# Optimization experiments

Measured on AMD Instinct MI355X. Metric: run time of the kernel, lower is better.

The kernel has to match this reference:

```python
import jax, jax.numpy as jnp
import numpy as np


def setup_inputs() -> dict:
    key = jax.random.key(0)
    k1, k2 = jax.random.split(key)
    x = jax.random.normal(k1, (16384, 4096), dtype=jnp.float32)
    # parameter initialized uniform(-0.01, 0.01) in the original
    v = jax.random.uniform(k2, (4096, 256), dtype=jnp.float32, minval=-0.01, maxval=0.01)
    return {"x": x, "v": v}


def reference(x, v):
    # FM second-order term: sum_{i<j} (v_i . v_j) x_i x_j
    # = 0.5 * (||x @ v||^2 - sum_f (x^2 @ v^2)_f), per batch row.
    xv = jnp.einsum('bn,nf->bf', x, v)            # [B, F]
    x2v2 = jnp.einsum('bn,nf->bf', x * x, v * v)  # [B, F]
    res = 0.5 * jnp.sum(xv * xv - x2v2, axis=-1, keepdims=True)  # [B, 1]
    return res
```

## Files before the change

kernel.cpp:

```cpp
#include <hip/hip_runtime.h>
#include <hip/hip_bf16.h>

#define B_DIM 16384
#define K_DIM 4096
#define F_DIM 256
#define BM 32
#define BK 64
#define NSTEP (K_DIM / BK)

typedef short bf16x8 __attribute__((ext_vector_type(8)));
typedef float f32x4 __attribute__((ext_vector_type(4)));

static __device__ __forceinline__ ushort f2bf(float f) {
    union { __hip_bfloat16 h; ushort s; } u;
    u.h = __float2bfloat16(f);
    return u.s;
}

static __device__ __forceinline__ void gload_lds16(const void* g, void* l) {
    __builtin_amdgcn_global_load_lds(
        (const __attribute__((address_space(1))) unsigned int*)g,
        (__attribute__((address_space(3))) unsigned int*)l, 16, 0, 0);
}

__global__ __launch_bounds__(512) void prep_w(const float* __restrict__ v,
                                              float* __restrict__ w) {
    const int lane = threadIdx.x & 63;
    const int n = blockIdx.x * 8 + (threadIdx.x >> 6);
    const float4 vv = *reinterpret_cast<const float4*>(v + (size_t)n * F_DIM + lane * 4);
    float s = vv.x * vv.x + vv.y * vv.y + vv.z * vv.z + vv.w * vv.w;
#pragma unroll
    for (int m = 1; m < 64; m <<= 1) s += __shfl_xor(s, m);
    if (lane == 0) w[n] = s;
}

__global__ __launch_bounds__(512) void prep_t(const float* __restrict__ v,
                                              ushort* __restrict__ vT) {
    __shared__ ushort T[256][72];
    const int tid = threadIdx.x;
    const int n0 = blockIdx.x * 64;
    const int wid = tid >> 6;
    const int f0 = (tid & 63) * 4;
#pragma unroll
    for (int j = 0; j < 8; ++j) {
        const int r = j * 8 + wid;
        const float4 vv = *reinterpret_cast<const float4*>(v + (size_t)(n0 + r) * F_DIM + f0);
        T[f0 + 0][r] = f2bf(vv.x);
        T[f0 + 1][r] = f2bf(vv.y);
        T[f0 + 2][r] = f2bf(vv.z);
        T[f0 + 3][r] = f2bf(vv.w);
    }
    __syncthreads();
    const int nb = (tid & 7) * 8;
#pragma unroll
    for (int s = 0; s < 4; ++s) {
        const int f = s * 64 + (tid >> 3);
        const uint4 val = *reinterpret_cast<const uint4*>(&T[f][nb]);
        *reinterpret_cast<uint4*>(vT + (size_t)f * K_DIM + n0 + nb) = val;
    }
}

__global__ __launch_bounds__(256, 3) void fm_kernel(const float* __restrict__ x,
                                                    const ushort* __restrict__ vT,
                                                    const float* __restrict__ w,
                                                    float* __restrict__ out) {
    __shared__ float Ab[2][BM * BK];
    __shared__ float red[BM][4];
    __shared__ float s2red[BM];

    const int tid = threadIdx.x;
    const int lane = tid & 63;
    const int wc = tid >> 6;
    const int l15 = lane & 15;
    const int koff = lane >> 4;

    const int mbase = blockIdx.x * BM;

    const int srow = tid >> 4;
    const int sj = (tid & 15) * 16;
    const int sjj = sj ^ ((srow & 7) << 4);
    const float* gx1 = x + (size_t)(mbase + srow) * K_DIM + (sjj >> 2);
    const float* gx2 = x + (size_t)(mbase + 16 + srow) * K_DIM + (sjj >> 2);

    auto stageA = [&](int k0, int buf) {
        char* base = reinterpret_cast<char*>(&Ab[buf][0]) + wc * 1024;
        gload_lds16(gx1 + k0, base);
        gload_lds16(gx2 + k0, base + 4096);
    };

    int aRo[2], aXm[2];
#pragma unroll
    for (int m = 0; m < 2; ++m) {
        const int r = m * 16 + l15;
        aRo[m] = r * 256;
        aXm[m] = (r & 7) << 4;
    }
    const int cbase = koff * 32;

    const ushort* vb = vT + (size_t)(wc * 64 + l15) * K_DIM + koff * 8;
    const float* wb = w + koff * 8;

    f32x4 acc[2][4] = {};
    float s2m0 = 0.f, s2m1 = 0.f;
    bf16x8 bA[4][2], bB[4][2];

    auto loadB = [&](int k0, bf16x8 (&bn)[4][2]) {
#pragma unroll
        for (int n = 0; n < 4; ++n)
#pragma unroll
            for (int ks = 0; ks < 2; ++ks)
                bn[n][ks] = *reinterpret_cast<const bf16x8*>(
                    vb + (size_t)n * 16 * K_DIM + k0 + ks * 32);
    };

    auto compute = [&](int k0, int buf, bf16x8 (&bc)[4][2]) {
        const char* Ac = reinterpret_cast<const char*>(&Ab[buf][0]);
        bf16x8 af[2][2];
#pragma unroll
        for (int ks = 0; ks < 2; ++ks) {
            float4 wlo = {0, 0, 0, 0}, whi = {0, 0, 0, 0};
            if (wc == 0) {
                wlo = *reinterpret_cast<const float4*>(wb + k0 + ks * 32);
                whi = *reinterpret_cast<const float4*>(wb + k0 + ks * 32 + 4);
            }
#pragma unroll
            for (int m = 0; m < 2; ++m) {
                const int c0 = (ks * 128 + cbase) ^ aXm[m];
                const int c1 = (ks * 128 + cbase + 16) ^ aXm[m];
                const f32x4 lo = *reinterpret_cast<const f32x4*>(Ac + aRo[m] + c0);
                const f32x4 hi = *reinterpret_cast<const f32x4*>(Ac + aRo[m] + c1);
                bf16x8 a;
                a[0] = (short)f2bf(lo[0]); a[1] = (short)f2bf(lo[1]);
                a[2] = (short)f2bf(lo[2]); a[3] = (short)f2bf(lo[3]);
                a[4] = (short)f2bf(hi[0]); a[5] = (short)f2bf(hi[1]);
                a[6] = (short)f2bf(hi[2]); a[7] = (short)f2bf(hi[3]);
                af[m][ks] = a;
                if (wc == 0) {
                    const float t = lo[0] * lo[0] * wlo.x + lo[1] * lo[1] * wlo.y
                                  + lo[2] * lo[2] * wlo.z + lo[3] * lo[3] * wlo.w
                                  + hi[0] * hi[0] * whi.x + hi[1] * hi[1] * whi.y
                                  + hi[2] * hi[2] * whi.z + hi[3] * hi[3] * whi.w;
                    if (m == 0) s2m0 += t; else s2m1 += t;
                }
            }
        }
#pragma unroll
        for (int ks = 0; ks < 2; ++ks)
#pragma unroll
            for (int m = 0; m < 2; ++m)
#pragma unroll
                for (int n = 0; n < 4; ++n)
                    acc[m][n] = __builtin_amdgcn_mfma_f32_16x16x32_bf16(
                        af[m][ks], bc[n][ks], acc[m][n], 0, 0, 0);
    };

    stageA(0, 0);
    loadB(0, bA);
    __syncthreads();

    for (int t = 0; t < NSTEP; t += 2) {
        stageA((t + 1) * BK, 1);
        loadB((t + 1) * BK, bB);
        compute(t * BK, 0, bA);
        __syncthreads();
        if (t + 2 < NSTEP) {
            stageA((t + 2) * BK, 0);
            loadB((t + 2) * BK, bA);
        }
        compute((t + 1) * BK, 1, bB);
        __syncthreads();
    }

#pragma unroll
    for (int m = 0; m < 2; ++m) {
#pragma unroll
        for (int j = 0; j < 4; ++j) {
            float s = 0.f;
#pragma unroll
            for (int n = 0; n < 4; ++n) { const float y = acc[m][n][j]; s += y * y; }
            s += __shfl_xor(s, 1);
            s += __shfl_xor(s, 2);
            s += __shfl_xor(s, 4);
            s += __shfl_xor(s, 8);
            if (l15 == 0) red[m * 16 + koff * 4 + j][wc] = s;
        }
    }
    if (wc == 0) {
        s2m0 += __shfl_xor(s2m0, 16); s2m0 += __shfl_xor(s2m0, 32);
        s2m1 += __shfl_xor(s2m1, 16); s2m1 += __shfl_xor(s2m1, 32);
        if (lane < 16) { s2red[lane] = s2m0; s2red[16 + lane] = s2m1; }
    }
    __syncthreads();
    if (tid < BM) {
        out[mbase + tid] = 0.5f * (red[tid][0] + red[tid][1] + red[tid][2]
                                   + red[tid][3] - s2red[tid]);
    }
}

extern "C" void kernel_launch(void* const* d_in, const int* in_sizes, int n_in,
                              void* d_out, int out_size, void* d_ws, size_t ws_size,
                              hipStream_t stream) {
    const float* x = (const float*)d_in[0];
    const float* v = (const float*)d_in[1];
    float* out = (float*)d_out;

    ushort* vT = (ushort*)d_ws;
    float* w = (float*)((char*)d_ws + (size_t)F_DIM * K_DIM * sizeof(ushort));

    prep_w<<<K_DIM / 8, 512, 0, stream>>>(v, w);
    prep_t<<<K_DIM / 64, 512, 0, stream>>>(v, vT);
    fm_kernel<<<B_DIM / BM, 256, 0, stream>>>(x, vT, w, out);
}
```

Measured before the change: 472.4 us.

## Stage A tile through registers as bf16 and spread x²·w work across all waves

Drops the direct global-to-LDS fp32 loads. Each thread now loads its x slice and w into registers two steps ahead, computes the x²·w partial sum, converts x to bf16 and writes packed, swizzled bf16 into LDS. The MFMA loop then reads bf16 fragments straight from LDS with no conversion, and the diagonal-term work is split over all four waves instead of only wave 0. In exchange it uses more registers for the prefetch buffers, and launch bounds drop occupancy from 3 to 2 blocks per SM; it also replaces __syncthreads with a manual waitcnt plus barrier.

```diff
diff --git a/kernel.cpp b/kernel.cpp
--- a/kernel.cpp
+++ b/kernel.cpp
@@ -15,12 +15,6 @@
     union { __hip_bfloat16 h; ushort s; } u;
     u.h = __float2bfloat16(f);
     return u.s;
-}
-
-static __device__ __forceinline__ void gload_lds16(const void* g, void* l) {
-    __builtin_amdgcn_global_load_lds(
-        (const __attribute__((address_space(1))) unsigned int*)g,
-        (__attribute__((address_space(3))) unsigned int*)l, 16, 0, 0);
 }
 
 __global__ __launch_bounds__(512) void prep_w(const float* __restrict__ v,
@@ -60,11 +54,14 @@
     }
 }
 
-__global__ __launch_bounds__(256, 3) void fm_kernel(const float* __restrict__ x,
+struct APend { float4 xa, xb, wa, wb; };
+struct BReg { bf16x8 v[4][2]; };
+
+__global__ __launch_bounds__(256, 2) void fm_kernel(const float* __restrict__ x,
                                                     const ushort* __restrict__ vT,
                                                     const float* __restrict__ w,
                                                     float* __restrict__ out) {
-    __shared__ float Ab[2][BM * BK];
+    __shared__ ushort As[2][BM * BK];
     __shared__ float red[BM][4];
     __shared__ float s2red[BM];
 
@@ -73,77 +70,64 @@
     const int wc = tid >> 6;
     const int l15 = lane & 15;
     const int koff = lane >> 4;
-
     const int mbase = blockIdx.x * BM;
 
-    const int srow = tid >> 4;
-    const int sj = (tid & 15) * 16;
-    const int sjj = sj ^ ((srow & 7) << 4);
-    const float* gx1 = x + (size_t)(mbase + srow) * K_DIM + (sjj >> 2);
-    const float* gx2 = x + (size_t)(mbase + 16 + srow) * K_DIM + (sjj >> 2);
-
-    auto stageA = [&](int k0, int buf) {
-        char* base = reinterpret_cast<char*>(&Ab[buf][0]) + wc * 1024;
-        gload_lds16(gx1 + k0, base);
-        gload_lds16(gx2 + k0, base + 4096);
-    };
-
-    int aRo[2], aXm[2];
-#pragma unroll
-    for (int m = 0; m < 2; ++m) {
-        const int r = m * 16 + l15;
-        aRo[m] = r * 256;
-        aXm[m] = (r & 7) << 4;
-    }
-    const int cbase = koff * 32;
-
+    const int srow = tid >> 3;
+    const int kb = (tid & 7) * 8;
+    const float* px = x + (size_t)(mbase + srow) * K_DIM + kb;
+    const float* pw = w + kb;
+    const int wbyte = srow * 128 + (((tid & 7) * 16) ^ ((srow & 7) << 4));
+
+    int aoff[2][2];
+#pragma unroll
+    for (int m = 0; m < 2; ++m)
+#pragma unroll
+        for (int ks = 0; ks < 2; ++ks)
+            aoff[m][ks] = (m * 16 + l15) * 128
+                        + ((koff * 16 + ks * 64) ^ ((l15 & 7) << 4));
     const ushort* vb = vT + (size_t)(wc * 64 + l15) * K_DIM + koff * 8;
-    const float* wb = w + koff * 8;
-
+
+    float s2 = 0.f;
     f32x4 acc[2][4] = {};
-    float s2m0 = 0.f, s2m1 = 0.f;
-    bf16x8 bA[4][2], bB[4][2];
-
-    auto loadB = [&](int k0, bf16x8 (&bn)[4][2]) {
+    APend p0, p1;
+    BReg b0, b1;
+
+    auto loadA = [&](int t, APend& p) {
+        const int k0 = (t < NSTEP ? t : NSTEP - 1) * BK;
+        p.xa = *reinterpret_cast<const float4*>(px + k0);
+        p.xb = *reinterpret_cast<const float4*>(px + k0 + 4);
+        p.wa = *reinterpret_cast<const float4*>(pw + k0);
+        p.wb = *reinterpret_cast<const float4*>(pw + k0 + 4);
+    };
+    auto loadB = [&](int t, BReg& b) {
+        const int k0 = (t < NSTEP ? t : NSTEP - 1) * BK;
 #pragma unroll
         for (int n = 0; n < 4; ++n)
 #pragma unroll
             for (int ks = 0; ks < 2; ++ks)
-                bn[n][ks] = *reinterpret_cast<const bf16x8*>(
+                b.v[n][ks] = *reinterpret_cast<const bf16x8*>(
                     vb + (size_t)n * 16 * K_DIM + k0 + ks * 32);
     };
-
-    auto compute = [&](int k0, int buf, bf16x8 (&bc)[4][2]) {
-        const char* Ac = reinterpret_cast<const char*>(&Ab[buf][0]);
+    auto writeA = [&](ushort* dst, const APend& p) {
+        s2 += p.xa.x * p.xa.x * p.wa.x + p.xa.y * p.xa.y * p.wa.y
+            + p.xa.z * p.xa.z * p.wa.z + p.xa.w * p.xa.w * p.wa.w
+            + p.xb.x * p.xb.x * p.wb.x + p.xb.y * p.xb.y * p.wb.y
+            + p.xb.z * p.xb.z * p.wb.z + p.xb.w * p.xb.w * p.wb.w;
+        uint4 pk;
+        pk.x = (uint)f2bf(p.xa.x) | ((uint)f2bf(p.xa.y) << 16);
+        pk.y = (uint)f2bf(p.xa.z) | ((uint)f2bf(p.xa.w) << 16);
+        pk.z = (uint)f2bf(p.xb.x) | ((uint)f2bf(p.xb.y) << 16);
+        pk.w = (uint)f2bf(p.xb.z) | ((uint)f2bf(p.xb.w) << 16);
+        *reinterpret_cast<uint4*>(reinterpret_cast<char*>(dst) + wbyte) = pk;
+    };
+    auto compute = [&](const ushort* Asrc, const BReg& b) {
+        const char* Ac = reinterpret_cast<const char*>(Asrc);
         bf16x8 af[2][2];
 #pragma unroll
-        for (int ks = 0; ks < 2; ++ks) {
-            float4 wlo = {0, 0, 0, 0}, whi = {0, 0, 0, 0};
-            if (wc == 0) {
-                wlo = *reinterpret_cast<const float4*>(wb + k0 + ks * 32);
-                whi = *reinterpret_cast<const float4*>(wb + k0 + ks * 32 + 4);
-            }
-#pragma unroll
-            for (int m = 0; m < 2; ++m) {
-                const int c0 = (ks * 128 + cbase) ^ aXm[m];
-                const int c1 = (ks * 128 + cbase + 16) ^ aXm[m];
-                const f32x4 lo = *reinterpret_cast<const f32x4*>(Ac + aRo[m] + c0);
-                const f32x4 hi = *reinterpret_cast<const f32x4*>(Ac + aRo[m] + c1);
-                bf16x8 a;
-                a[0] = (short)f2bf(lo[0]); a[1] = (short)f2bf(lo[1]);
-                a[2] = (short)f2bf(lo[2]); a[3] = (short)f2bf(lo[3]);
-                a[4] = (short)f2bf(hi[0]); a[5] = (short)f2bf(hi[1]);
-                a[6] = (short)f2bf(hi[2]); a[7] = (short)f2bf(hi[3]);
-                af[m][ks] = a;
-                if (wc == 0) {
-                    const float t = lo[0] * lo[0] * wlo.x + lo[1] * lo[1] * wlo.y
-                                  + lo[2] * lo[2] * wlo.z + lo[3] * lo[3] * wlo.w
-                                  + hi[0] * hi[0] * whi.x + hi[1] * hi[1] * whi.y
-                                  + hi[2] * hi[2] * whi.z + hi[3] * hi[3] * whi.w;
-                    if (m == 0) s2m0 += t; else s2m1 += t;
-                }
-            }
-        }
+        for (int m = 0; m < 2; ++m)
+#pragma unroll
+            for (int ks = 0; ks < 2; ++ks)
+                af[m][ks] = *reinterpret_cast<const bf16x8*>(Ac + aoff[m][ks]);
 #pragma unroll
         for (int ks = 0; ks < 2; ++ks)
 #pragma unroll
@@ -151,24 +135,32 @@
 #pragma unroll
                 for (int n = 0; n < 4; ++n)
                     acc[m][n] = __builtin_amdgcn_mfma_f32_16x16x32_bf16(
-                        af[m][ks], bc[n][ks], acc[m][n], 0, 0, 0);
-    };
-
-    stageA(0, 0);
-    loadB(0, bA);
-    __syncthreads();
+                        af[m][ks], b.v[n][ks], acc[m][n], 0, 0, 0);
+    };
+
+    loadA(0, p0);
+    loadA(1, p1);
+    loadB(0, b0);
+    writeA(As[0], p0);
+    asm volatile("s_waitcnt lgkmcnt(0)" ::: "memory");
+    __builtin_amdgcn_s_barrier();
 
     for (int t = 0; t < NSTEP; t += 2) {
-        stageA((t + 1) * BK, 1);
-        loadB((t + 1) * BK, bB);
-        compute(t * BK, 0, bA);
-        __syncthreads();
-        if (t + 2 < NSTEP) {
-            stageA((t + 2) * BK, 0);
-            loadB((t + 2) * BK, bA);
-        }
-        compute((t + 1) * BK, 1, bB);
-        __syncthreads();
+        loadA(t + 2, p0);
+        loadB(t + 1, b1);
+        asm volatile("" ::: "memory");
+        compute(As[0], b0);
+        if (t + 1 < NSTEP) writeA(As[1], p1);
+        asm volatile("s_waitcnt lgkmcnt(0)" ::: "memory");
+        __builtin_amdgcn_s_barrier();
+
+        loadA(t + 3, p1);
+        loadB(t + 2, b0);
+        asm volatile("" ::: "memory");
+        compute(As[1], b1);
+        if (t + 2 < NSTEP) writeA(As[0], p0);
+        asm volatile("s_waitcnt lgkmcnt(0)" ::: "memory");
+        __builtin_amdgcn_s_barrier();
     }
 
 #pragma unroll
@@ -185,11 +177,10 @@
             if (l15 == 0) red[m * 16 + koff * 4 + j][wc] = s;
         }
     }
-    if (wc == 0) {
-        s2m0 += __shfl_xor(s2m0, 16); s2m0 += __shfl_xor(s2m0, 32);
-        s2m1 += __shfl_xor(s2m1, 16); s2m1 += __shfl_xor(s2m1, 32);
-        if (lane < 16) { s2red[lane] = s2m0; s2red[16 + lane] = s2m1; }
-    }
+    s2 += __shfl_xor(s2, 1);
+    s2 += __shfl_xor(s2, 2);
+    s2 += __shfl_xor(s2, 4);
+    if ((tid & 7) == 0) s2red[srow] = s2;
     __syncthreads();
     if (tid < BM) {
         out[mbase + tid] = 0.5f * (red[tid][0] + red[tid][1] + red[tid][2]
```

Result: faster. 424.5 us (-10.1%).
